# Kernel optimization log

Measured on AMD Instinct MI355X. Metric: run time of the kernel, lower is better.

The kernel has to match this reference:

```python
import jax, jax.numpy as jnp
import numpy as np

THRESHOLD = 0.02  # matches init threshold
N_POINTS = 4_000_000
N_PLANES = 64


def setup_inputs() -> dict:
    key = jax.random.key(0)
    k1, k2, k3 = jax.random.split(key, 3)
    points = jax.random.uniform(k1, (N_POINTS, 3), dtype=jnp.float32)
    normals = jax.random.normal(k2, (N_PLANES, 3), dtype=jnp.float32)
    normals = normals / jnp.linalg.norm(normals, axis=1, keepdims=True)
    # anchor each plane at a random point inside the cube so it intersects the cloud
    anchors = jax.random.uniform(k3, (N_PLANES, 3), dtype=jnp.float32)
    distances = jnp.sum(normals * anchors, axis=1)
    return {"points": points, "normals": normals, "distances": distances}


def reference(points, normals, distances):
    """Sequential per-plane SVD refinement + masked projection (faithful to torch loop).

    Plane fits (mask, centroid, covariance) use the ORIGINAL points, as in the
    source; only the projection is applied cumulatively to the running state.
    """
    dtype = points.dtype
    jitter = jnp.diag(jnp.asarray([1.0, 2.0, 3.0], dtype))  # keeps eigh well-posed for invalid planes

    def step(proj, plane):
        n, d = plane
        # inlier mask on original points (data-dependent in torch; here a weight vector)
        m = (jnp.abs(points @ n - d) < THRESHOLD).astype(dtype)  # (N,)
        cnt = jnp.sum(m)
        validf = (cnt >= 3.0).astype(dtype)
        centroid = jnp.sum(m[:, None] * points, axis=0) / jnp.maximum(cnt, 1.0)  # (3,)
        xc = (points - centroid) * m[:, None]  # masked centered points (N,3)
        cov = xc.T @ xc  # (3,3), m is 0/1 so single weighting == mask-select
        cov = cov + (1.0 - validf) * jitter
        # smallest-eigenvalue eigenvector of symmetric cov == torch V[:, 2] (up to sign)
        _, V = jnp.linalg.eigh(cov)
        rn = V[:, 0]
        rn = jnp.where(jnp.dot(rn, n) < 0.0, -rn, rn)  # align with coarse normal
        rd = jnp.dot(centroid, rn)
        # project only masked points of the running state onto refined plane
        delta = (proj @ rn - rd)[:, None] * rn[None, :]  # (N,3)
        proj = proj - (validf * m)[:, None] * delta
        return proj, None

    proj, _ = jax.lax.scan(step, points, (normals, distances))
    return proj
```

## Files before the change

### kernel.cpp

```cpp
#include <hip/hip_runtime.h>
#include <math.h>

#define N_POINTS 4000000
#define N_PLANES 64
#define THRESH   0.02f
#define NVALS    (N_PLANES*10)
#define PPT      16
#define BLKPTS   (PPT*64)
#define G1       1024
#define ITEMS    4
#define NPB      (G1*ITEMS)
#define NPAD     (NPB*BLKPTS - N_POINTS)
#define FULL_PB  (N_POINTS/BLKPTS)
#define SEG_R    16
#define RTHR     256

__device__ __forceinline__ float bperm(int addr, float v) {
    return __uint_as_float(__builtin_amdgcn_ds_bpermute(addr, __float_as_uint(v)));
}

__global__ __launch_bounds__(RTHR, 4)
void reduce_kernel(const float* __restrict__ pts,
                   const float* __restrict__ nrm,
                   const float* __restrict__ dst,
                   float* __restrict__ partials)
{
    const int lane = threadIdx.x & 63;
    const int wid  = threadIdx.x >> 6;

    __shared__ float part[RTHR/64][NVALS];

    const int rotaddr = ((lane + 1) & 63) << 2;

    float cnx, cny, cnz, cnd;
    {
        const int q = (lane + SEG_R * wid) & 63;
        cnx = nrm[q*3+0]; cny = nrm[q*3+1]; cnz = nrm[q*3+2]; cnd = -dst[q];
    }

    float a0=0.f,a1=0.f,a2=0.f,a3=0.f,a4=0.f,a5=0.f,a6=0.f,a7=0.f,a8=0.f,a9=0.f;
    float PX[PPT], PY[PPT], PZ[PPT];

    for (int it = 0; it < ITEMS; ++it) {
        const int pb = blockIdx.x * ITEMS + it;

        const float* P0 = pts + ((size_t)pb * BLKPTS + lane) * 3;
        if (pb < FULL_PB) {
#pragma unroll
            for (int u = 0; u < PPT; ++u) {
                PX[u] = P0[u*192+0]; PY[u] = P0[u*192+1]; PZ[u] = P0[u*192+2];
            }
        } else if (pb == FULL_PB) {
#pragma unroll
            for (int u = 0; u < PPT; ++u) {
                if (u < 4) { PX[u] = P0[u*192+0]; PY[u] = P0[u*192+1]; PZ[u] = P0[u*192+2]; }
                else       { PX[u] = 0.f; PY[u] = 0.f; PZ[u] = 0.f; }
            }
        } else {
#pragma unroll
            for (int u = 0; u < PPT; ++u) { PX[u] = 0.f; PY[u] = 0.f; PZ[u] = 0.f; }
        }

#pragma unroll 1
        for (int r = 0; r < SEG_R; ++r) {
#pragma unroll
            for (int u = 0; u < PPT; ++u) {
                const float x = PX[u], y = PY[u], z = PZ[u];
                const float t  = fmaf(x, cnx, fmaf(y, cny, fmaf(z, cnz, cnd)));
                const bool  m  = fabsf(t) < THRESH;
                const float fm = m ? 1.0f : 0.0f;
                const float tx = m ? x : 0.0f;
                const float ty = m ? y : 0.0f;
                const float tz = m ? z : 0.0f;
                a0 += fm;
                a1 += tx; a2 += ty; a3 += tz;
                a4 = fmaf(tx, x, a4); a5 = fmaf(tx, y, a5); a6 = fmaf(tx, z, a6);
                a7 = fmaf(ty, y, a7); a8 = fmaf(ty, z, a8); a9 = fmaf(tz, z, a9);
            }
            cnx = bperm(rotaddr, cnx); cny = bperm(rotaddr, cny);
            cnz = bperm(rotaddr, cnz); cnd = bperm(rotaddr, cnd);
            a0 = bperm(rotaddr, a0); a1 = bperm(rotaddr, a1);
            a2 = bperm(rotaddr, a2); a3 = bperm(rotaddr, a3);
            a4 = bperm(rotaddr, a4); a5 = bperm(rotaddr, a5);
            a6 = bperm(rotaddr, a6); a7 = bperm(rotaddr, a7);
            a8 = bperm(rotaddr, a8); a9 = bperm(rotaddr, a9);
        }
    }

    {
        const int wp = (lane + SEG_R * wid) & 63;
        float* rr = &part[wid][wp * 10];
        rr[0]=a0; rr[1]=a1; rr[2]=a2; rr[3]=a3; rr[4]=a4;
        rr[5]=a5; rr[6]=a6; rr[7]=a7; rr[8]=a8; rr[9]=a9;
    }
    __syncthreads();
    for (int v = threadIdx.x; v < NVALS; v += RTHR) {
        float sum = 0.f;
#pragma unroll
        for (int ww = 0; ww < RTHR/64; ++ww) sum += part[ww][v];
        partials[(long long)blockIdx.x * NVALS + v] = sum;
    }
}

__global__ __launch_bounds__(256)
void finalize_kernel(const float* __restrict__ partials, int nb,
                     const float* __restrict__ nrm,
                     const float* __restrict__ dst,
                     float* __restrict__ params)
{
    const int p    = blockIdx.x;
    const int lane = threadIdx.x & 63;
    const int wid  = threadIdx.x >> 6;

    double s[10];
#pragma unroll
    for (int q = 0; q < 10; ++q) s[q] = 0.0;

    for (int b = threadIdx.x; b < nb; b += 256) {
        const float* row = partials + (long long)b * NVALS + p * 10;
#pragma unroll
        for (int q = 0; q < 10; ++q) s[q] += (double)row[q];
    }

#pragma unroll
    for (int off = 32; off; off >>= 1)
#pragma unroll
        for (int q = 0; q < 10; ++q) s[q] += __shfl_xor(s[q], off);

    __shared__ double wsum[4][10];
    if (lane == 0) {
#pragma unroll
        for (int q = 0; q < 10; ++q) wsum[wid][q] = s[q];
    }
    __syncthreads();
    if (threadIdx.x != 0) return;

    double acc[10];
#pragma unroll
    for (int q = 0; q < 10; ++q)
        acc[q] = wsum[0][q] + wsum[1][q] + wsum[2][q] + wsum[3][q];

    double cnt = acc[0];
    if (fabsf(dst[p]) < THRESH) cnt -= (double)NPAD;

    const double sx = acc[1], sy = acc[2], sz = acc[3];
    const double den = fmax(cnt, 1.0);
    const double cx = sx / den, cy = sy / den, cz = sz / den;

    double C[3][3];
    C[0][0] = acc[4] - 2.0*cx*sx + cnt*cx*cx;
    C[0][1] = acc[5] - cx*sy - cy*sx + cnt*cx*cy;
    C[0][2] = acc[6] - cx*sz - cz*sx + cnt*cx*cz;
    C[1][1] = acc[7] - 2.0*cy*sy + cnt*cy*cy;
    C[1][2] = acc[8] - cy*sz - cz*sy + cnt*cy*cz;
    C[2][2] = acc[9] - 2.0*cz*sz + cnt*cz*cz;
    C[1][0] = C[0][1]; C[2][0] = C[0][2]; C[2][1] = C[1][2];

    const double valid = (cnt >= 3.0) ? 1.0 : 0.0;
    C[0][0] += (1.0 - valid) * 1.0;
    C[1][1] += (1.0 - valid) * 2.0;
    C[2][2] += (1.0 - valid) * 3.0;

    double V[3][3] = {{1,0,0},{0,1,0},{0,0,1}};
    for (int sweep = 0; sweep < 15; ++sweep) {
#pragma unroll
        for (int k = 0; k < 3; ++k) {
            const int pp = (k == 2) ? 1 : 0;
            const int qq = (k == 0) ? 1 : 2;
            const int rr = 3 - pp - qq;
            const double apq = C[pp][qq];
            if (fabs(apq) < 1e-300) continue;
            const double theta = (C[qq][qq] - C[pp][pp]) / (2.0 * apq);
            const double t = copysign(1.0, theta) / (fabs(theta) + sqrt(theta*theta + 1.0));
            const double c = 1.0 / sqrt(t*t + 1.0);
            const double ss = t * c;
            const double app = C[pp][pp], aqq = C[qq][qq];
            const double arp = C[rr][pp], arq = C[rr][qq];
            C[pp][pp] = app - t * apq;
            C[qq][qq] = aqq + t * apq;
            C[pp][qq] = 0.0; C[qq][pp] = 0.0;
            const double nrp = c*arp - ss*arq;
            const double nrq = ss*arp + c*arq;
            C[rr][pp] = nrp; C[pp][rr] = nrp;
            C[rr][qq] = nrq; C[qq][rr] = nrq;
#pragma unroll
            for (int i = 0; i < 3; ++i) {
                const double vip = V[i][pp], viq = V[i][qq];
                V[i][pp] = c*vip - ss*viq;
                V[i][qq] = ss*vip + c*viq;
            }
        }
    }

    int idx = 0;
    if (C[1][1] < C[idx][idx]) idx = 1;
    if (C[2][2] < C[idx][idx]) idx = 2;
    double rx = V[0][idx], ry = V[1][idx], rz = V[2][idx];
    const double inv = 1.0 / sqrt(rx*rx + ry*ry + rz*rz);
    rx *= inv; ry *= inv; rz *= inv;

    const double nxd = (double)nrm[p*3+0];
    const double nyd = (double)nrm[p*3+1];
    const double nzd = (double)nrm[p*3+2];
    if (rx*nxd + ry*nyd + rz*nzd < 0.0) { rx = -rx; ry = -ry; rz = -rz; }
    const double rd = cx*rx + cy*ry + cz*rz;

    const float vldf = (float)valid;
    params[p*8+0] = nrm[p*3+0];
    params[p*8+1] = nrm[p*3+1];
    params[p*8+2] = nrm[p*3+2];
    params[p*8+3] = -dst[p];
    params[p*8+4] = vldf * (float)rx;
    params[p*8+5] = vldf * (float)ry;
    params[p*8+6] = vldf * (float)rz;
    params[p*8+7] = -(vldf * (float)rd);
}

#define PPTH 8
#define PQ   (N_POINTS / PPTH)

__global__ __launch_bounds__(256)
void project_kernel(const float* __restrict__ pts,
                    const float* __restrict__ params,
                    float* __restrict__ out)
{
    const int tid = blockIdx.x * 256 + threadIdx.x;
    if (tid >= PQ) return;

    float ox[PPTH], oy[PPTH], oz[PPTH];
    float qx[PPTH], qy[PPTH], qz[PPTH];
#pragma unroll
    for (int k = 0; k < PPTH; ++k) {
        const long long i = (long long)tid + (long long)k * PQ;
        ox[k] = pts[i*3+0]; oy[k] = pts[i*3+1]; oz[k] = pts[i*3+2];
        qx[k] = ox[k]; qy[k] = oy[k]; qz[k] = oz[k];
    }

#pragma unroll 2
    for (int p = 0; p < N_PLANES; ++p) {
        const float nx  = params[p*8+0];
        const float ny  = params[p*8+1];
        const float nz  = params[p*8+2];
        const float md  = params[p*8+3];
        const float rvx = params[p*8+4];
        const float rvy = params[p*8+5];
        const float rvz = params[p*8+6];
        const float mrd = params[p*8+7];

#pragma unroll
        for (int k = 0; k < PPTH; ++k) {
            const float t0 = fmaf(ox[k], nx, fmaf(oy[k], ny, fmaf(oz[k], nz, md)));
            const float t  = fmaf(qx[k], rvx, fmaf(qy[k], rvy, fmaf(qz[k], rvz, mrd)));
            const float tm = (fabsf(t0) < THRESH) ? t : 0.0f;
            qx[k] = fmaf(-tm, rvx, qx[k]);
            qy[k] = fmaf(-tm, rvy, qy[k]);
            qz[k] = fmaf(-tm, rvz, qz[k]);
        }
    }

#pragma unroll
    for (int k = 0; k < PPTH; ++k) {
        const long long i = (long long)tid + (long long)k * PQ;
        out[i*3+0] = qx[k];
        out[i*3+1] = qy[k];
        out[i*3+2] = qz[k];
    }
}

extern "C" void kernel_launch(void* const* d_in, const int* in_sizes, int n_in,
                              void* d_out, int out_size, void* d_ws, size_t ws_size,
                              hipStream_t stream)
{
    const float* pts = (const float*)d_in[0];
    const float* nrm = (const float*)d_in[1];
    const float* dst = (const float*)d_in[2];
    float* out = (float*)d_out;

    float* partials = (float*)d_ws;
    size_t poff = ((size_t)G1 * NVALS * sizeof(float) + 255) & ~(size_t)255;
    float* params = (float*)((char*)d_ws + poff);

    hipLaunchKernelGGL(reduce_kernel, dim3(G1), dim3(RTHR), 0, stream,
                       pts, nrm, dst, partials);
    hipLaunchKernelGGL(finalize_kernel, dim3(N_PLANES), dim3(256), 0, stream,
                       partials, G1, nrm, dst, params);
    hipLaunchKernelGGL(project_kernel, dim3((PQ + 255) / 256), dim3(256), 0, stream,
                       pts, params, out);
}
```

Before: 197.0 us.

## Use packed FP32 math with branchless clamp-based inlier mask in reduce and project

```diff
diff --git a/kernel.cpp b/kernel.cpp
--- a/kernel.cpp
+++ b/kernel.cpp
@@ -6,6 +6,7 @@
 #define THRESH   0.02f
 #define NVALS    (N_PLANES*10)
 #define PPT      16
+#define NPAIR    (PPT/2)
 #define BLKPTS   (PPT*64)
 #define G1       1024
 #define ITEMS    4
@@ -15,6 +16,23 @@
 #define SEG_R    16
 #define RTHR     256
 
+typedef float v2f __attribute__((ext_vector_type(2)));
+
+__device__ __forceinline__ v2f pk_fma(v2f a, v2f b, v2f c) {
+    v2f d; asm("v_pk_fma_f32 %0, %1, %2, %3" : "=v"(d) : "v"(a), "v"(b), "v"(c)); return d;
+}
+__device__ __forceinline__ v2f pk_mul(v2f a, v2f b) {
+    v2f d; asm("v_pk_mul_f32 %0, %1, %2" : "=v"(d) : "v"(a), "v"(b)); return d;
+}
+__device__ __forceinline__ v2f pk_mul_clamp(v2f a, v2f b) {
+    v2f d; asm("v_pk_mul_f32 %0, %1, %2 clamp" : "=v"(d) : "v"(a), "v"(b)); return d;
+}
+__device__ __forceinline__ void pk_adda(v2f& acc, v2f a) {
+    asm("v_pk_add_f32 %0, %1, %0" : "+v"(acc) : "v"(a));
+}
+__device__ __forceinline__ void pk_fmaa(v2f& acc, v2f a, v2f b) {
+    asm("v_pk_fma_f32 %0, %1, %2, %0" : "+v"(acc) : "v"(a), "v"(b));
+}
 __device__ __forceinline__ float bperm(int addr, float v) {
     return __uint_as_float(__builtin_amdgcn_ds_bpermute(addr, __float_as_uint(v)));
 }
@@ -32,66 +50,85 @@
 
     const int rotaddr = ((lane + 1) & 63) << 2;
 
-    float cnx, cny, cnz, cnd;
+    const v2f TH2N2 = { -(THRESH*THRESH), -(THRESH*THRESH) };
+    const v2f NBIG2 = { -1e20f, -1e20f };
+
+    v2f nx2, ny2, nz2, nd2;
     {
         const int q = (lane + SEG_R * wid) & 63;
-        cnx = nrm[q*3+0]; cny = nrm[q*3+1]; cnz = nrm[q*3+2]; cnd = -dst[q];
-    }
-
-    float a0=0.f,a1=0.f,a2=0.f,a3=0.f,a4=0.f,a5=0.f,a6=0.f,a7=0.f,a8=0.f,a9=0.f;
-    float PX[PPT], PY[PPT], PZ[PPT];
+        const float a = nrm[q*3+0], b = nrm[q*3+1], c = nrm[q*3+2], d = -dst[q];
+        nx2 = (v2f){a,a}; ny2 = (v2f){b,b}; nz2 = (v2f){c,c}; nd2 = (v2f){d,d};
+    }
+
+    v2f a2[10];
+#pragma unroll
+    for (int i = 0; i < 10; ++i) a2[i] = (v2f){0.f, 0.f};
+
+    v2f PX2[NPAIR], PY2[NPAIR], PZ2[NPAIR];
 
     for (int it = 0; it < ITEMS; ++it) {
         const int pb = blockIdx.x * ITEMS + it;
-
         const float* P0 = pts + ((size_t)pb * BLKPTS + lane) * 3;
+
         if (pb < FULL_PB) {
 #pragma unroll
-            for (int u = 0; u < PPT; ++u) {
-                PX[u] = P0[u*192+0]; PY[u] = P0[u*192+1]; PZ[u] = P0[u*192+2];
+            for (int v = 0; v < NPAIR; ++v) {
+                PX2[v] = (v2f){ P0[(2*v)*192+0], P0[(2*v+1)*192+0] };
+                PY2[v] = (v2f){ P0[(2*v)*192+1], P0[(2*v+1)*192+1] };
+                PZ2[v] = (v2f){ P0[(2*v)*192+2], P0[(2*v+1)*192+2] };
             }
         } else if (pb == FULL_PB) {
 #pragma unroll
-            for (int u = 0; u < PPT; ++u) {
-                if (u < 4) { PX[u] = P0[u*192+0]; PY[u] = P0[u*192+1]; PZ[u] = P0[u*192+2]; }
-                else       { PX[u] = 0.f; PY[u] = 0.f; PZ[u] = 0.f; }
+            for (int v = 0; v < NPAIR; ++v) {
+                if (v < 2) {
+                    PX2[v] = (v2f){ P0[(2*v)*192+0], P0[(2*v+1)*192+0] };
+                    PY2[v] = (v2f){ P0[(2*v)*192+1], P0[(2*v+1)*192+1] };
+                    PZ2[v] = (v2f){ P0[(2*v)*192+2], P0[(2*v+1)*192+2] };
+                } else {
+                    PX2[v] = (v2f){0.f,0.f}; PY2[v] = (v2f){0.f,0.f}; PZ2[v] = (v2f){0.f,0.f};
+                }
             }
         } else {
 #pragma unroll
-            for (int u = 0; u < PPT; ++u) { PX[u] = 0.f; PY[u] = 0.f; PZ[u] = 0.f; }
+            for (int v = 0; v < NPAIR; ++v) {
+                PX2[v] = (v2f){0.f,0.f}; PY2[v] = (v2f){0.f,0.f}; PZ2[v] = (v2f){0.f,0.f};
+            }
         }
 
 #pragma unroll 1
         for (int r = 0; r < SEG_R; ++r) {
 #pragma unroll
-            for (int u = 0; u < PPT; ++u) {
-                const float x = PX[u], y = PY[u], z = PZ[u];
-                const float t  = fmaf(x, cnx, fmaf(y, cny, fmaf(z, cnz, cnd)));
-                const bool  m  = fabsf(t) < THRESH;
-                const float fm = m ? 1.0f : 0.0f;
-                const float tx = m ? x : 0.0f;
-                const float ty = m ? y : 0.0f;
-                const float tz = m ? z : 0.0f;
-                a0 += fm;
-                a1 += tx; a2 += ty; a3 += tz;
-                a4 = fmaf(tx, x, a4); a5 = fmaf(tx, y, a5); a6 = fmaf(tx, z, a6);
-                a7 = fmaf(ty, y, a7); a8 = fmaf(ty, z, a8); a9 = fmaf(tz, z, a9);
-            }
-            cnx = bperm(rotaddr, cnx); cny = bperm(rotaddr, cny);
-            cnz = bperm(rotaddr, cnz); cnd = bperm(rotaddr, cnd);
-            a0 = bperm(rotaddr, a0); a1 = bperm(rotaddr, a1);
-            a2 = bperm(rotaddr, a2); a3 = bperm(rotaddr, a3);
-            a4 = bperm(rotaddr, a4); a5 = bperm(rotaddr, a5);
-            a6 = bperm(rotaddr, a6); a7 = bperm(rotaddr, a7);
-            a8 = bperm(rotaddr, a8); a9 = bperm(rotaddr, a9);
+            for (int v = 0; v < NPAIR; ++v) {
+                const v2f t2  = pk_fma(PX2[v], nx2, pk_fma(PY2[v], ny2, pk_fma(PZ2[v], nz2, nd2)));
+                const v2f d2  = pk_fma(t2, t2, TH2N2);
+                const v2f fm2 = pk_mul_clamp(d2, NBIG2);
+                const v2f tx2 = pk_mul(PX2[v], fm2);
+                const v2f ty2 = pk_mul(PY2[v], fm2);
+                const v2f tz2 = pk_mul(PZ2[v], fm2);
+                pk_adda(a2[0], fm2);
+                pk_adda(a2[1], tx2); pk_adda(a2[2], ty2); pk_adda(a2[3], tz2);
+                pk_fmaa(a2[4], tx2, PX2[v]); pk_fmaa(a2[5], tx2, PY2[v]); pk_fmaa(a2[6], tx2, PZ2[v]);
+                pk_fmaa(a2[7], ty2, PY2[v]); pk_fmaa(a2[8], ty2, PZ2[v]); pk_fmaa(a2[9], tz2, PZ2[v]);
+            }
+            float s[10];
+#pragma unroll
+            for (int i = 0; i < 10; ++i) s[i] = a2[i].x + a2[i].y;
+#pragma unroll
+            for (int i = 0; i < 10; ++i) s[i] = bperm(rotaddr, s[i]);
+#pragma unroll
+            for (int i = 0; i < 10; ++i) a2[i] = (v2f){ s[i], 0.f };
+            nx2.x = bperm(rotaddr, nx2.x); nx2.y = nx2.x;
+            ny2.x = bperm(rotaddr, ny2.x); ny2.y = ny2.x;
+            nz2.x = bperm(rotaddr, nz2.x); nz2.y = nz2.x;
+            nd2.x = bperm(rotaddr, nd2.x); nd2.y = nd2.x;
         }
     }
 
     {
         const int wp = (lane + SEG_R * wid) & 63;
         float* rr = &part[wid][wp * 10];
-        rr[0]=a0; rr[1]=a1; rr[2]=a2; rr[3]=a3; rr[4]=a4;
-        rr[5]=a5; rr[6]=a6; rr[7]=a7; rr[8]=a8; rr[9]=a9;
+#pragma unroll
+        for (int i = 0; i < 10; ++i) rr[i] = a2[i].x + a2[i].y;
     }
     __syncthreads();
     for (int v = threadIdx.x; v < NVALS; v += RTHR) {
@@ -141,7 +178,7 @@
         acc[q] = wsum[0][q] + wsum[1][q] + wsum[2][q] + wsum[3][q];
 
     double cnt = acc[0];
-    if (fabsf(dst[p]) < THRESH) cnt -= (double)NPAD;
+    if (fmaf(dst[p], dst[p], -(THRESH*THRESH)) < 0.0f) cnt -= (double)NPAD;
 
     const double sx = acc[1], sy = acc[2], sz = acc[3];
     const double den = fmax(cnt, 1.0);
@@ -227,13 +264,19 @@
     const int tid = blockIdx.x * 256 + threadIdx.x;
     if (tid >= PQ) return;
 
-    float ox[PPTH], oy[PPTH], oz[PPTH];
-    float qx[PPTH], qy[PPTH], qz[PPTH];
-#pragma unroll
-    for (int k = 0; k < PPTH; ++k) {
-        const long long i = (long long)tid + (long long)k * PQ;
-        ox[k] = pts[i*3+0]; oy[k] = pts[i*3+1]; oz[k] = pts[i*3+2];
-        qx[k] = ox[k]; qy[k] = oy[k]; qz[k] = oz[k];
+    const v2f TH2N2 = { -(THRESH*THRESH), -(THRESH*THRESH) };
+    const v2f NBIG2 = { -1e20f, -1e20f };
+    const v2f NEG12 = { -1.f, -1.f };
+
+    v2f ox2[4], oy2[4], oz2[4], qx2[4], qy2[4], qz2[4];
+#pragma unroll
+    for (int k = 0; k < 4; ++k) {
+        const long long i0 = (long long)tid + (long long)(2*k)   * PQ;
+        const long long i1 = (long long)tid + (long long)(2*k+1) * PQ;
+        ox2[k] = (v2f){ pts[i0*3+0], pts[i1*3+0] };
+        oy2[k] = (v2f){ pts[i0*3+1], pts[i1*3+1] };
+        oz2[k] = (v2f){ pts[i0*3+2], pts[i1*3+2] };
+        qx2[k] = ox2[k]; qy2[k] = oy2[k]; qz2[k] = oz2[k];
     }
 
 #pragma unroll 2
@@ -246,24 +289,29 @@
         const float rvy = params[p*8+5];
         const float rvz = params[p*8+6];
         const float mrd = params[p*8+7];
-
-#pragma unroll
-        for (int k = 0; k < PPTH; ++k) {
-            const float t0 = fmaf(ox[k], nx, fmaf(oy[k], ny, fmaf(oz[k], nz, md)));
-            const float t  = fmaf(qx[k], rvx, fmaf(qy[k], rvy, fmaf(qz[k], rvz, mrd)));
-            const float tm = (fabsf(t0) < THRESH) ? t : 0.0f;
-            qx[k] = fmaf(-tm, rvx, qx[k]);
-            qy[k] = fmaf(-tm, rvy, qy[k]);
-            qz[k] = fmaf(-tm, rvz, qz[k]);
+        const v2f nx2  = (v2f){nx,nx},   ny2  = (v2f){ny,ny},   nz2 = (v2f){nz,nz};
+        const v2f md2  = (v2f){md,md},   mrd2 = (v2f){mrd,mrd};
+        const v2f rvx2 = (v2f){rvx,rvx}, rvy2 = (v2f){rvy,rvy}, rvz2 = (v2f){rvz,rvz};
+
+#pragma unroll
+        for (int k = 0; k < 4; ++k) {
+            const v2f t0  = pk_fma(ox2[k], nx2, pk_fma(oy2[k], ny2, pk_fma(oz2[k], nz2, md2)));
+            const v2f d2  = pk_fma(t0, t0, TH2N2);
+            const v2f fm2 = pk_mul_clamp(d2, NBIG2);
+            const v2f tt  = pk_fma(qx2[k], rvx2, pk_fma(qy2[k], rvy2, pk_fma(qz2[k], rvz2, mrd2)));
+            const v2f ftn = pk_mul(pk_mul(tt, fm2), NEG12);
+            qx2[k] = pk_fma(ftn, rvx2, qx2[k]);
+            qy2[k] = pk_fma(ftn, rvy2, qy2[k]);
+            qz2[k] = pk_fma(ftn, rvz2, qz2[k]);
         }
     }
 
 #pragma unroll
-    for (int k = 0; k < PPTH; ++k) {
-        const long long i = (long long)tid + (long long)k * PQ;
-        out[i*3+0] = qx[k];
-        out[i*3+1] = qy[k];
-        out[i*3+2] = qz[k];
+    for (int k = 0; k < 4; ++k) {
+        const long long i0 = (long long)tid + (long long)(2*k)   * PQ;
+        const long long i1 = (long long)tid + (long long)(2*k+1) * PQ;
+        out[i0*3+0] = qx2[k].x; out[i0*3+1] = qy2[k].x; out[i0*3+2] = qz2[k].x;
+        out[i1*3+0] = qx2[k].y; out[i1*3+1] = qy2[k].y; out[i1*3+2] = qz2[k].y;
     }
 }
 
```

Measured after the change: 181.3 us. 8.0% less time.
